# Performance work log

Hardware: AMD Instinct MI355X
Metric: run time of the kernel (lower is better)

The kernel has to match this reference:

```python
import jax, jax.numpy as jnp
import numpy as np

B, S, HID = 2, 2048, 2048
H, HKV, DH = 32, 8, 64
GROUPS = H // HKV
SCALE = DH ** -0.5
ROPE_THETA = 10000.0
NEG_INF = jnp.finfo(jnp.float32).min


def setup_inputs() -> dict:
    key = jax.random.key(0)
    ks = jax.random.split(key, 6)
    hidden_states = jax.random.normal(ks[0], (B, S, HID), dtype=jnp.float32)
    # true rotary embeddings (HF Llama style): inv_freq over half dim, duplicated
    inv_freq = 1.0 / (ROPE_THETA ** (np.arange(0, DH, 2, dtype=np.float32) / DH))
    freqs = np.arange(S, dtype=np.float32)[:, None] * inv_freq[None, :]  # [S, DH/2]
    emb = np.concatenate([freqs, freqs], axis=-1)                        # [S, DH]
    cos = jnp.broadcast_to(jnp.asarray(np.cos(emb), jnp.float32), (B, S, DH))
    sin = jnp.broadcast_to(jnp.asarray(np.sin(emb), jnp.float32), (B, S, DH))
    # additive causal mask [1,1,S,S]
    causal = jnp.tril(jnp.ones((S, S), dtype=bool))
    attention_mask = jnp.where(causal, 0.0, NEG_INF)[None, None].astype(jnp.float32)
    std = 0.02
    Wq = jax.random.normal(ks[1], (H * DH, HID), dtype=jnp.float32) * std
    Wk = jax.random.normal(ks[2], (HKV * DH, HID), dtype=jnp.float32) * std
    Wv = jax.random.normal(ks[3], (HKV * DH, HID), dtype=jnp.float32) * std
    Wo = jax.random.normal(ks[4], (HID, H * DH), dtype=jnp.float32) * std
    return {"hidden_states": hidden_states, "cos": cos, "sin": sin,
            "attention_mask": attention_mask, "Wq": Wq, "Wk": Wk, "Wv": Wv, "Wo": Wo}


def _rotate_half(x):
    x1, x2 = jnp.split(x, 2, axis=-1)
    return jnp.concatenate([-x2, x1], axis=-1)


def reference(hidden_states, cos, sin, attention_mask, Wq, Wk, Wv, Wo):
    b, s, _ = hidden_states.shape
    # projections -> [B, H(kv), S, DH]
    q = (hidden_states @ Wq.T).reshape(b, s, H, DH).transpose(0, 2, 1, 3)
    k = (hidden_states @ Wk.T).reshape(b, s, HKV, DH).transpose(0, 2, 1, 3)
    v = (hidden_states @ Wv.T).reshape(b, s, HKV, DH).transpose(0, 2, 1, 3)
    # RoPE (cos/sin: [B,S,DH] -> broadcast over head axis)
    c = cos[:, None, :, :]
    sn = sin[:, None, :, :]
    q = q * c + _rotate_half(q) * sn
    k = k * c + _rotate_half(k) * sn
    # GQA: repeat kv heads
    k = jnp.repeat(k, GROUPS, axis=1)  # [B,H,S,DH]
    v = jnp.repeat(v, GROUPS, axis=1)
    # eager attention: full [B,H,S,S] scores in memory
    scores = jnp.einsum('bhqd,bhkd->bhqk', q, k) * SCALE + attention_mask[:, :, :, :s]
    attn = jax.nn.softmax(scores, axis=-1)
    out = jnp.einsum('bhqk,bhkd->bhqd', attn, v)
    out = out.transpose(0, 2, 1, 3).reshape(b, s, H * DH)
    return out @ Wo.T
```

## Files before the change

kernel.cpp:

```cpp
#include <hip/hip_runtime.h>
#include <hip/hip_bf16.h>
#include <cstdint>
#include <cstddef>

#define B_    2
#define S_    2048
#define HID_  2048
#define H_    32
#define HKV_  8
#define DH_   64
#define SC2_  0.1803368801111244f

typedef __bf16 bf16;
typedef bf16  bf16x2 __attribute__((ext_vector_type(2)));
typedef bf16  bf16x4 __attribute__((ext_vector_type(4)));
typedef bf16  bf16x8 __attribute__((ext_vector_type(8)));
typedef float f32x4  __attribute__((ext_vector_type(4)));
typedef float f32x16 __attribute__((ext_vector_type(16)));
typedef uint32_t u32x2 __attribute__((ext_vector_type(2)));

typedef __attribute__((address_space(3))) uint32_t  lds_u32_t;
typedef __attribute__((address_space(1))) const uint32_t glob_u32_t;

__device__ __forceinline__ void async16(const void* g, void* l) {
    __builtin_amdgcn_global_load_lds((glob_u32_t*)g, (lds_u32_t*)l, 16, 0, 0);
}

__device__ __forceinline__ bf16x8 cvt8(float4 a, float4 b) {
    bf16x8 r;
    r[0] = (bf16)a.x; r[1] = (bf16)a.y; r[2] = (bf16)a.z; r[3] = (bf16)a.w;
    r[4] = (bf16)b.x; r[5] = (bf16)b.y; r[6] = (bf16)b.z; r[7] = (bf16)b.w;
    return r;
}

__device__ __forceinline__ uint32_t pkbf(float a, float b) {
    bf16x2 t; t[0] = (bf16)a; t[1] = (bf16)b;
    return __builtin_bit_cast(uint32_t, t);
}
__device__ __forceinline__ bf16x8 mk8(uint32_t a, uint32_t b, uint32_t c, uint32_t d) {
    union { uint32_t u[4]; bf16x8 v; } t;
    t.u[0] = a; t.u[1] = b; t.u[2] = c; t.u[3] = d;
    return t.v;
}

__global__ __launch_bounds__(256) void cvt_all_kernel(
    const float* __restrict__ X,  const float* __restrict__ Wq,
    const float* __restrict__ Wk, const float* __restrict__ Wv,
    const float* __restrict__ Wo,
    bf16* __restrict__ Xb,  bf16* __restrict__ Wqb, bf16* __restrict__ Wkb,
    bf16* __restrict__ Wvb, bf16* __restrict__ Wob)
{
    const int i = blockIdx.x * 256 + threadIdx.x;
    const float* src; bf16* dst; int off;
    if (i < 1048576)      { src = X;  dst = Xb;  off = i; }
    else if (i < 1572864) { src = Wq; dst = Wqb; off = i - 1048576; }
    else if (i < 1703936) { src = Wk; dst = Wkb; off = i - 1572864; }
    else if (i < 1835008) { src = Wv; dst = Wvb; off = i - 1703936; }
    else                  { src = Wo; dst = Wob; off = i - 1835008; }
    float4 a = ((const float4*)src)[2 * off];
    float4 b = ((const float4*)src)[2 * off + 1];
    ((bf16x8*)dst)[off] = cvt8(a, b);
}

__global__ __launch_bounds__(256) void gemm_qkv_kernel(
    const bf16* __restrict__ A,
    const bf16* __restrict__ Wqb, const bf16* __restrict__ Wkb,
    const bf16* __restrict__ Wvb,
    const float* __restrict__ cs, const float* __restrict__ sn,
    bf16* __restrict__ Qo, bf16* __restrict__ Ko, bf16* __restrict__ Vt)
{
    __shared__ bf16 a_lds[128 * 64];
    __shared__ bf16 b_lds[128 * 64];

    const int tid  = threadIdx.x;
    const int wave = tid >> 6;
    const int lane = tid & 63;
    const int quad = lane >> 4;
    const int l16  = lane & 15;
    const int wm   = wave >> 1;
    const int wn   = wave & 1;
    const int m0   = blockIdx.x * 128;
    const int n0   = blockIdx.y * 128;

    f32x4 acc[4][4];
    #pragma unroll
    for (int mt = 0; mt < 4; ++mt)
        #pragma unroll
        for (int nt = 0; nt < 4; ++nt)
            acc[mt][nt] = (f32x4){0.f, 0.f, 0.f, 0.f};

    int srow[4], sgcol[4];
    const bf16* browp[4];
    #pragma unroll
    for (int i = 0; i < 4; ++i) {
        const int e = tid * 8 + i * 2048;
        srow[i] = e >> 6;
        const int chunk = (e >> 3) & 7;
        sgcol[i] = (chunk ^ (srow[i] & 7)) << 3;
        const int n = n0 + srow[i];
        browp[i] = (n < 2048) ? (Wqb + (size_t)n * HID_)
                 : (n < 2560) ? (Wkb + (size_t)(n - 2048) * HID_)
                              : (Wvb + (size_t)(n - 2560) * HID_);
    }

    for (int k0 = 0; k0 < HID_; k0 += 64) {
        #pragma unroll
        for (int i = 0; i < 4; ++i) {
            async16(A + (size_t)(m0 + srow[i]) * HID_ + k0 + sgcol[i],
                    &a_lds[tid * 8 + i * 2048]);
            async16(browp[i] + k0 + sgcol[i],
                    &b_lds[tid * 8 + i * 2048]);
        }
        __syncthreads();
        #pragma unroll
        for (int ks = 0; ks < 2; ++ks) {
            bf16x8 af[4], bfr[4];
            #pragma unroll
            for (int mt = 0; mt < 4; ++mt) {
                const int row = wm * 64 + mt * 16 + l16;
                const int c = (ks * 4 + quad) ^ (row & 7);
                af[mt] = *(const bf16x8*)(&a_lds[row * 64 + c * 8]);
            }
            #pragma unroll
            for (int nt = 0; nt < 4; ++nt) {
                const int row = wn * 64 + nt * 16 + l16;
                const int c = (ks * 4 + quad) ^ (row & 7);
                bfr[nt] = *(const bf16x8*)(&b_lds[row * 64 + c * 8]);
            }
            #pragma unroll
            for (int mt = 0; mt < 4; ++mt)
                #pragma unroll
                for (int nt = 0; nt < 4; ++nt)
                    acc[mt][nt] = __builtin_amdgcn_mfma_f32_16x16x32_bf16(
                        af[mt], bfr[nt], acc[mt][nt], 0, 0, 0);
        }
        __syncthreads();
    }

    const int nw = n0 + wn * 64;
    const int d  = l16;
    #pragma unroll
    for (int mt = 0; mt < 4; ++mt) {
        #pragma unroll
        for (int r = 0; r < 4; ++r) {
            const int m  = m0 + wm * 64 + mt * 16 + quad * 4 + r;
            const int bb = m >> 11;
            const int ss = m & (S_ - 1);
            const float v0 = acc[mt][0][r], v1 = acc[mt][1][r];
            const float v2 = acc[mt][2][r], v3 = acc[mt][3][r];
            if (nw < 2048) {
                const int h = nw >> 6;
                bf16* dp = Qo + ((size_t)(bb * H_ + h) * S_ + ss) * DH_;
                const float* cp = cs + ((size_t)bb * S_ + ss) * DH_;
                const float* sp = sn + ((size_t)bb * S_ + ss) * DH_;
                dp[ 0 + d] = (bf16)((v0 * cp[ 0 + d] - v2 * sp[ 0 + d]) * SC2_);
                dp[16 + d] = (bf16)((v1 * cp[16 + d] - v3 * sp[16 + d]) * SC2_);
                dp[32 + d] = (bf16)((v2 * cp[32 + d] + v0 * sp[32 + d]) * SC2_);
                dp[48 + d] = (bf16)((v3 * cp[48 + d] + v1 * sp[48 + d]) * SC2_);
            } else if (nw < 2560) {
                const int h = (nw - 2048) >> 6;
                bf16* dp = Ko + ((size_t)(bb * HKV_ + h) * S_ + ss) * DH_;
                const float* cp = cs + ((size_t)bb * S_ + ss) * DH_;
                const float* sp = sn + ((size_t)bb * S_ + ss) * DH_;
                dp[ 0 + d] = (bf16)(v0 * cp[ 0 + d] - v2 * sp[ 0 + d]);
                dp[16 + d] = (bf16)(v1 * cp[16 + d] - v3 * sp[16 + d]);
                dp[32 + d] = (bf16)(v2 * cp[32 + d] + v0 * sp[32 + d]);
                dp[48 + d] = (bf16)(v3 * cp[48 + d] + v1 * sp[48 + d]);
            } else {
                const int h = (nw - 2560) >> 6;
                bf16* dp = Vt + ((size_t)(bb * HKV_ + h) * DH_) * S_ + ss;
                dp[(size_t)( 0 + d) * S_] = (bf16)v0;
                dp[(size_t)(16 + d) * S_] = (bf16)v1;
                dp[(size_t)(32 + d) * S_] = (bf16)v2;
                dp[(size_t)(48 + d) * S_] = (bf16)v3;
            }
        }
    }
}

__global__ __launch_bounds__(256) void gemm_out_kernel(
    const bf16* __restrict__ A, const bf16* __restrict__ Wb,
    float* __restrict__ Y)
{
    __shared__ bf16 a_lds[128 * 64];
    __shared__ bf16 b_lds[128 * 64];

    const int tid  = threadIdx.x;
    const int wave = tid >> 6;
    const int lane = tid & 63;
    const int quad = lane >> 4;
    const int l16  = lane & 15;
    const int wm   = wave >> 1;
    const int wn   = wave & 1;
    const int m0   = blockIdx.x * 128;
    const int n0   = blockIdx.y * 128;

    f32x4 acc[4][4];
    #pragma unroll
    for (int mt = 0; mt < 4; ++mt)
        #pragma unroll
        for (int nt = 0; nt < 4; ++nt)
            acc[mt][nt] = (f32x4){0.f, 0.f, 0.f, 0.f};

    int srow[4], sgcol[4];
    #pragma unroll
    for (int i = 0; i < 4; ++i) {
        const int e = tid * 8 + i * 2048;
        srow[i] = e >> 6;
        const int chunk = (e >> 3) & 7;
        sgcol[i] = (chunk ^ (srow[i] & 7)) << 3;
    }

    for (int k0 = 0; k0 < HID_; k0 += 64) {
        #pragma unroll
        for (int i = 0; i < 4; ++i) {
            async16(A + (size_t)(m0 + srow[i]) * HID_ + k0 + sgcol[i],
                    &a_lds[tid * 8 + i * 2048]);
            async16(Wb + (size_t)(n0 + srow[i]) * HID_ + k0 + sgcol[i],
                    &b_lds[tid * 8 + i * 2048]);
        }
        __syncthreads();
        #pragma unroll
        for (int ks = 0; ks < 2; ++ks) {
            bf16x8 af[4], bfr[4];
            #pragma unroll
            for (int mt = 0; mt < 4; ++mt) {
                const int row = wm * 64 + mt * 16 + l16;
                const int c = (ks * 4 + quad) ^ (row & 7);
                af[mt] = *(const bf16x8*)(&a_lds[row * 64 + c * 8]);
            }
            #pragma unroll
            for (int nt = 0; nt < 4; ++nt) {
                const int row = wn * 64 + nt * 16 + l16;
                const int c = (ks * 4 + quad) ^ (row & 7);
                bfr[nt] = *(const bf16x8*)(&b_lds[row * 64 + c * 8]);
            }
            #pragma unroll
            for (int mt = 0; mt < 4; ++mt)
                #pragma unroll
                for (int nt = 0; nt < 4; ++nt)
                    acc[mt][nt] = __builtin_amdgcn_mfma_f32_16x16x32_bf16(
                        af[mt], bfr[nt], acc[mt][nt], 0, 0, 0);
        }
        __syncthreads();
    }

    #pragma unroll
    for (int mt = 0; mt < 4; ++mt)
        #pragma unroll
        for (int nt = 0; nt < 4; ++nt)
            #pragma unroll
            for (int r = 0; r < 4; ++r) {
                const int m = m0 + wm * 64 + mt * 16 + quad * 4 + r;
                const int n = n0 + wn * 64 + nt * 16 + l16;
                Y[(size_t)m * HID_ + n] = acc[mt][nt][r];
            }
}

__global__ __launch_bounds__(256) void attn_kernel(
    const bf16* __restrict__ Q, const bf16* __restrict__ K,
    const bf16* __restrict__ Vt, bf16* __restrict__ O)
{
    __shared__ bf16 k_lds[2][64 * 64];
    __shared__ bf16 v_lds[2][64 * 64];

    const int tid  = threadIdx.x;
    const int wave = tid >> 6;
    const int lane = tid & 63;
    const int l32  = lane & 31;
    const int half = lane >> 5;
    const int h  = blockIdx.y;
    const int b  = blockIdx.z;
    const int hkv = h >> 2;

    const bf16* Qg = Q  + (size_t)(b * H_ + h) * S_ * DH_;
    const bf16* Kg = K  + (size_t)(b * HKV_ + hkv) * S_ * DH_;
    const bf16* Vg = Vt + ((size_t)(b * HKV_ + hkv) * DH_) * S_;

    const int srow0  = tid >> 3;
    const int scolsw = ((tid & 7) ^ ((tid >> 3) & 7)) << 3;

    const int p   = blockIdx.x;
    const int st  = (wave < 2) ? p : (31 - p);
    const int qb0 = st * 64 + (wave & 1) * 32;
    const int qa  = qb0 + l32;
    const int nkt = 32 - p;

    bf16x8 qf[4];
    #pragma unroll
    for (int c = 0; c < 4; ++c)
        qf[c] = *(const bf16x8*)(Qg + (size_t)qa * DH_ + c * 16 + half * 8);

    f32x16 o_acc[2];
    #pragma unroll
    for (int dt = 0; dt < 2; ++dt)
        #pragma unroll
        for (int e = 0; e < 16; ++e) o_acc[dt][e] = 0.f;
    float m_i = -1e30f, l_i = 0.f;

    #pragma unroll
    for (int i = 0; i < 2; ++i) {
        const int row = srow0 + i * 32;
        async16(Kg + (size_t)row * DH_ + scolsw, &k_lds[0][tid * 8 + i * 2048]);
        async16(Vg + (size_t)row * S_  + scolsw, &v_lds[0][tid * 8 + i * 2048]);
    }
    __syncthreads();

    for (int kt = 0; kt < nkt; ++kt) {
        if (kt + 1 < nkt) {
            bf16* kb = k_lds[(kt + 1) & 1];
            bf16* vb = v_lds[(kt + 1) & 1];
            #pragma unroll
            for (int i = 0; i < 2; ++i) {
                const int row = srow0 + i * 32;
                async16(Kg + (size_t)((kt + 1) * 64 + row) * DH_ + scolsw,
                        kb + tid * 8 + i * 2048);
                async16(Vg + (size_t)row * S_ + (kt + 1) * 64 + scolsw,
                        vb + tid * 8 + i * 2048);
            }
        }

        if (kt * 64 <= qb0 + 31) {
            const bf16* kb = k_lds[kt & 1];
            const bf16* vb = v_lds[kt & 1];
            const bool act1 = (kt * 64 + 32) <= (qb0 + 31);

            f32x16 s0, s1;
            {
                bf16x8 kf[4];
                #pragma unroll
                for (int c = 0; c < 4; ++c) {
                    const int row = l32;
                    const int col = ((2 * c + half) ^ (row & 7)) << 3;
                    kf[c] = *(const bf16x8*)(kb + row * 64 + col);
                }
                f32x16 a;
                #pragma unroll
                for (int e = 0; e < 16; ++e) a[e] = 0.f;
                #pragma unroll
                for (int c = 0; c < 4; ++c)
                    a = __builtin_amdgcn_mfma_f32_32x32x16_bf16(kf[c], qf[c], a, 0, 0, 0);
                s0 = a;
            }
            if (act1) {
                bf16x8 kf[4];
                #pragma unroll
                for (int c = 0; c < 4; ++c) {
                    const int row = 32 + l32;
                    const int col = ((2 * c + half) ^ (row & 7)) << 3;
                    kf[c] = *(const bf16x8*)(kb + row * 64 + col);
                }
                f32x16 a;
                #pragma unroll
                for (int e = 0; e < 16; ++e) a[e] = 0.f;
                #pragma unroll
                for (int c = 0; c < 4; ++c)
                    a = __builtin_amdgcn_mfma_f32_32x32x16_bf16(kf[c], qf[c], a, 0, 0, 0);
                s1 = a;
            }

            if (!((kt * 64 + 31) <= qb0)) {
                const int qrel = qa - kt * 64 - 4 * half;
                #pragma unroll
                for (int e = 0; e < 16; ++e)
                    if (((e & 3) + 8 * (e >> 2)) > qrel) s0[e] = -1e30f;
            }
            if (act1 && !((kt * 64 + 63) <= qb0)) {
                const int qrel = qa - kt * 64 - 32 - 4 * half;
                #pragma unroll
                for (int e = 0; e < 16; ++e)
                    if (((e & 3) + 8 * (e >> 2)) > qrel) s1[e] = -1e30f;
            }

            float mx = s0[0];
            #pragma unroll
            for (int e = 1; e < 16; ++e) mx = fmaxf(mx, s0[e]);
            if (act1)
                #pragma unroll
                for (int e = 0; e < 16; ++e) mx = fmaxf(mx, s1[e]);
            mx = fmaxf(mx, __shfl_xor(mx, 32));

            float al = 1.f;
            if (!__all(mx <= m_i + 8.f)) {
                const float mn = fmaxf(m_i, mx);
                al = exp2f(m_i - mn);
                m_i = mn;
                #pragma unroll
                for (int dt = 0; dt < 2; ++dt)
                    #pragma unroll
                    for (int e = 0; e < 16; ++e) o_acc[dt][e] *= al;
            }

            float sm = 0.f;
            #pragma unroll
            for (int e = 0; e < 16; ++e) {
                const float pp = exp2f(s0[e] - m_i);
                s0[e] = pp; sm += pp;
            }
            if (act1)
                #pragma unroll
                for (int e = 0; e < 16; ++e) {
                    const float pp = exp2f(s1[e] - m_i);
                    s1[e] = pp; sm += pp;
                }
            sm += __shfl_xor(sm, 32);
            l_i = l_i * al + sm;

            bf16x8 pf[4];
            {
                uint32_t d0 = pkbf(s0[0],  s0[1]),  d1 = pkbf(s0[2],  s0[3]);
                uint32_t d2 = pkbf(s0[4],  s0[5]),  d3 = pkbf(s0[6],  s0[7]);
                uint32_t d4 = pkbf(s0[8],  s0[9]),  d5 = pkbf(s0[10], s0[11]);
                uint32_t d6 = pkbf(s0[12], s0[13]), d7 = pkbf(s0[14], s0[15]);
                u32x2 r02 = __builtin_amdgcn_permlane32_swap(d0, d2, false, false);
                u32x2 r13 = __builtin_amdgcn_permlane32_swap(d1, d3, false, false);
                u32x2 r46 = __builtin_amdgcn_permlane32_swap(d4, d6, false, false);
                u32x2 r57 = __builtin_amdgcn_permlane32_swap(d5, d7, false, false);
                pf[0] = mk8(r02[0], r13[0], r02[1], r13[1]);
                pf[1] = mk8(r46[0], r57[0], r46[1], r57[1]);
            }
            if (act1) {
                uint32_t d0 = pkbf(s1[0],  s1[1]),  d1 = pkbf(s1[2],  s1[3]);
                uint32_t d2 = pkbf(s1[4],  s1[5]),  d3 = pkbf(s1[6],  s1[7]);
                uint32_t d4 = pkbf(s1[8],  s1[9]),  d5 = pkbf(s1[10], s1[11]);
                uint32_t d6 = pkbf(s1[12], s1[13]), d7 = pkbf(s1[14], s1[15]);
                u32x2 r02 = __builtin_amdgcn_permlane32_swap(d0, d2, false, false);
                u32x2 r13 = __builtin_amdgcn_permlane32_swap(d1, d3, false, false);
                u32x2 r46 = __builtin_amdgcn_permlane32_swap(d4, d6, false, false);
                u32x2 r57 = __builtin_amdgcn_permlane32_swap(d5, d7, false, false);
                pf[2] = mk8(r02[0], r13[0], r02[1], r13[1]);
                pf[3] = mk8(r46[0], r57[0], r46[1], r57[1]);
            }

            bf16x8 vf[2][4];
            #pragma unroll
            for (int dt = 0; dt < 2; ++dt)
                #pragma unroll
                for (int c = 0; c < 4; ++c) {
                    const int row = dt * 32 + l32;
                    const int col = ((2 * c + half) ^ (row & 7)) << 3;
                    vf[dt][c] = *(const bf16x8*)(vb + row * 64 + col);
                }

            const int nc = act1 ? 4 : 2;
            #pragma unroll
            for (int c = 0; c < 4; ++c) {
                if (c >= nc) break;
                #pragma unroll
                for (int dt = 0; dt < 2; ++dt)
                    o_acc[dt] = __builtin_amdgcn_mfma_f32_32x32x16_bf16(
                        vf[dt][c], pf[c], o_acc[dt], 0, 0, 0);
            }
        }
        __syncthreads();
    }

    const float inv = 1.f / l_i;
    bf16* op = O + ((size_t)(b * S_ + qa) * H_ + h) * DH_;
    #pragma unroll
    for (int dt = 0; dt < 2; ++dt)
        #pragma unroll
        for (int g = 0; g < 4; ++g) {
            bf16x4 ov;
            #pragma unroll
            for (int r = 0; r < 4; ++r) ov[r] = (bf16)(o_acc[dt][g * 4 + r] * inv);
            *(bf16x4*)(op + dt * 32 + g * 8 + half * 4) = ov;
        }
}

extern "C" void kernel_launch(void* const* d_in, const int* in_sizes, int n_in,
                              void* d_out, int out_size, void* d_ws, size_t ws_size,
                              hipStream_t stream)
{
    const float* X    = (const float*)d_in[0];
    const float* cs   = (const float*)d_in[1];
    const float* sn   = (const float*)d_in[2];
    const float* Wq   = (const float*)d_in[4];
    const float* Wk   = (const float*)d_in[5];
    const float* Wv   = (const float*)d_in[6];
    const float* Wo   = (const float*)d_in[7];
    float* Y          = (float*)d_out;

    bf16* Xb  = (bf16*)d_ws;
    bf16* Wqb = Xb  + (size_t)8388608;
    bf16* Wkb = Wqb + (size_t)4194304;
    bf16* Wvb = Wkb + (size_t)1048576;
    bf16* Wob = Wvb + (size_t)1048576;
    bf16* Qb  = Wob + (size_t)4194304;
    bf16* Kb  = Qb  + (size_t)8388608;
    bf16* Vtb = Kb  + (size_t)2097152;
    bf16* Ob  = Vtb + (size_t)2097152;

    dim3 blk(256);
    cvt_all_kernel<<<dim3(9216), blk, 0, stream>>>(X, Wq, Wk, Wv, Wo,
                                                   Xb, Wqb, Wkb, Wvb, Wob);
    gemm_qkv_kernel<<<dim3(32, 24), blk, 0, stream>>>(Xb, Wqb, Wkb, Wvb,
                                                      cs, sn, Qb, Kb, Vtb);
    attn_kernel<<<dim3(16, H_, B_), blk, 0, stream>>>(Qb, Kb, Vtb, Ob);
    gemm_out_kernel<<<dim3(32, 16), blk, 0, stream>>>(Ob, Wob, Y);
}
```

Before: 418.3 us.

## Restructure attention to 128-row query tiles with 32-key KV tiles

The attention kernel moves from paired 64-row query tiles (front and back halves for causal balance) to one 128-row query tile per block, with each wave owning 32 rows. It streams K/V in 32-key tiles with a repacked V LDS layout, and uses a rotated block-to-tile mapping across heads and batches for load balance. Each K/V tile is now reused by four waves instead of two, and the smaller tiles halve LDS use and cut masked work on the diagonal. In exchange there are twice as many loop iterations and barriers per key range, and scheduling balance now relies on the rotation instead of explicit pairing.

```diff
diff --git a/kernel.cpp b/kernel.cpp
--- a/kernel.cpp
+++ b/kernel.cpp
@@ -261,8 +261,8 @@
     const bf16* __restrict__ Q, const bf16* __restrict__ K,
     const bf16* __restrict__ Vt, bf16* __restrict__ O)
 {
-    __shared__ bf16 k_lds[2][64 * 64];
-    __shared__ bf16 v_lds[2][64 * 64];
+    __shared__ bf16 k_lds[2][32 * 64];
+    __shared__ bf16 v_lds[2][32 * 64];
 
     const int tid  = threadIdx.x;
     const int wave = tid >> 6;
@@ -277,14 +277,16 @@
     const bf16* Kg = K  + (size_t)(b * HKV_ + hkv) * S_ * DH_;
     const bf16* Vg = Vt + ((size_t)(b * HKV_ + hkv) * DH_) * S_;
 
-    const int srow0  = tid >> 3;
-    const int scolsw = ((tid & 7) ^ ((tid >> 3) & 7)) << 3;
-
-    const int p   = blockIdx.x;
-    const int st  = (wave < 2) ? p : (31 - p);
-    const int qb0 = st * 64 + (wave & 1) * 32;
+    const int qt  = 15 - ((blockIdx.x + 4 * ((h >> 4) + 2 * b)) & 15);
+    const int qb0 = qt * 128 + wave * 32;
     const int qa  = qb0 + l32;
-    const int nkt = 32 - p;
+    const int nkt = 4 * qt + 4;
+
+    const int kr = tid >> 3;
+    const int kj = ((tid & 7) ^ (kr & 7)) << 3;
+    const int vj = (tid & 7) ^ (kr & 7);
+    const int vd = kr + 32 * (vj >> 2);
+    const int vs = (vj & 3) * 8;
 
     bf16x8 qf[4];
     #pragma unroll
@@ -298,41 +300,29 @@
         for (int e = 0; e < 16; ++e) o_acc[dt][e] = 0.f;
     float m_i = -1e30f, l_i = 0.f;
 
-    #pragma unroll
-    for (int i = 0; i < 2; ++i) {
-        const int row = srow0 + i * 32;
-        async16(Kg + (size_t)row * DH_ + scolsw, &k_lds[0][tid * 8 + i * 2048]);
-        async16(Vg + (size_t)row * S_  + scolsw, &v_lds[0][tid * 8 + i * 2048]);
-    }
+    async16(Kg + (size_t)kr * DH_ + kj,  &k_lds[0][tid * 8]);
+    async16(Vg + (size_t)vd * S_  + vs,  &v_lds[0][tid * 8]);
     __syncthreads();
 
     for (int kt = 0; kt < nkt; ++kt) {
         if (kt + 1 < nkt) {
-            bf16* kb = k_lds[(kt + 1) & 1];
-            bf16* vb = v_lds[(kt + 1) & 1];
-            #pragma unroll
-            for (int i = 0; i < 2; ++i) {
-                const int row = srow0 + i * 32;
-                async16(Kg + (size_t)((kt + 1) * 64 + row) * DH_ + scolsw,
-                        kb + tid * 8 + i * 2048);
-                async16(Vg + (size_t)row * S_ + (kt + 1) * 64 + scolsw,
-                        vb + tid * 8 + i * 2048);
-            }
-        }
-
-        if (kt * 64 <= qb0 + 31) {
+            async16(Kg + (size_t)((kt + 1) * 32 + kr) * DH_ + kj,
+                    &k_lds[(kt + 1) & 1][tid * 8]);
+            async16(Vg + (size_t)vd * S_ + (kt + 1) * 32 + vs,
+                    &v_lds[(kt + 1) & 1][tid * 8]);
+        }
+
+        if (kt * 32 <= qb0 + 31) {
             const bf16* kb = k_lds[kt & 1];
             const bf16* vb = v_lds[kt & 1];
-            const bool act1 = (kt * 64 + 32) <= (qb0 + 31);
-
-            f32x16 s0, s1;
+
+            f32x16 s0;
             {
                 bf16x8 kf[4];
                 #pragma unroll
                 for (int c = 0; c < 4; ++c) {
-                    const int row = l32;
-                    const int col = ((2 * c + half) ^ (row & 7)) << 3;
-                    kf[c] = *(const bf16x8*)(kb + row * 64 + col);
+                    const int ch = (2 * c + half) ^ (l32 & 7);
+                    kf[c] = *(const bf16x8*)(kb + l32 * 64 + ch * 8);
                 }
                 f32x16 a;
                 #pragma unroll
@@ -342,42 +332,17 @@
                     a = __builtin_amdgcn_mfma_f32_32x32x16_bf16(kf[c], qf[c], a, 0, 0, 0);
                 s0 = a;
             }
-            if (act1) {
-                bf16x8 kf[4];
-                #pragma unroll
-                for (int c = 0; c < 4; ++c) {
-                    const int row = 32 + l32;
-                    const int col = ((2 * c + half) ^ (row & 7)) << 3;
-                    kf[c] = *(const bf16x8*)(kb + row * 64 + col);
-                }
-                f32x16 a;
-                #pragma unroll
-                for (int e = 0; e < 16; ++e) a[e] = 0.f;
-                #pragma unroll
-                for (int c = 0; c < 4; ++c)
-                    a = __builtin_amdgcn_mfma_f32_32x32x16_bf16(kf[c], qf[c], a, 0, 0, 0);
-                s1 = a;
-            }
-
-            if (!((kt * 64 + 31) <= qb0)) {
-                const int qrel = qa - kt * 64 - 4 * half;
+
+            if (!((kt * 32 + 31) <= qb0)) {
+                const int qrel = qa - kt * 32 - 4 * half;
                 #pragma unroll
                 for (int e = 0; e < 16; ++e)
                     if (((e & 3) + 8 * (e >> 2)) > qrel) s0[e] = -1e30f;
             }
-            if (act1 && !((kt * 64 + 63) <= qb0)) {
-                const int qrel = qa - kt * 64 - 32 - 4 * half;
-                #pragma unroll
-                for (int e = 0; e < 16; ++e)
-                    if (((e & 3) + 8 * (e >> 2)) > qrel) s1[e] = -1e30f;
-            }
 
             float mx = s0[0];
             #pragma unroll
             for (int e = 1; e < 16; ++e) mx = fmaxf(mx, s0[e]);
-            if (act1)
-                #pragma unroll
-                for (int e = 0; e < 16; ++e) mx = fmaxf(mx, s1[e]);
             mx = fmaxf(mx, __shfl_xor(mx, 32));
 
             float al = 1.f;
@@ -397,16 +362,10 @@
                 const float pp = exp2f(s0[e] - m_i);
                 s0[e] = pp; sm += pp;
             }
-            if (act1)
-                #pragma unroll
-                for (int e = 0; e < 16; ++e) {
-                    const float pp = exp2f(s1[e] - m_i);
-                    s1[e] = pp; sm += pp;
-                }
             sm += __shfl_xor(sm, 32);
             l_i = l_i * al + sm;
 
-            bf16x8 pf[4];
+            bf16x8 pf[2];
             {
                 uint32_t d0 = pkbf(s0[0],  s0[1]),  d1 = pkbf(s0[2],  s0[3]);
                 uint32_t d2 = pkbf(s0[4],  s0[5]),  d3 = pkbf(s0[6],  s0[7]);
@@ -419,38 +378,22 @@
                 pf[0] = mk8(r02[0], r13[0], r02[1], r13[1]);
                 pf[1] = mk8(r46[0], r57[0], r46[1], r57[1]);
             }
-            if (act1) {
-                uint32_t d0 = pkbf(s1[0],  s1[1]),  d1 = pkbf(s1[2],  s1[3]);
-                uint32_t d2 = pkbf(s1[4],  s1[5]),  d3 = pkbf(s1[6],  s1[7]);
-                uint32_t d4 = pkbf(s1[8],  s1[9]),  d5 = pkbf(s1[10], s1[11]);
-                uint32_t d6 = pkbf(s1[12], s1[13]), d7 = pkbf(s1[14], s1[15]);
-                u32x2 r02 = __builtin_amdgcn_permlane32_swap(d0, d2, false, false);
-                u32x2 r13 = __builtin_amdgcn_permlane32_swap(d1, d3, false, false);
-                u32x2 r46 = __builtin_amdgcn_permlane32_swap(d4, d6, false, false);
-                u32x2 r57 = __builtin_amdgcn_permlane32_swap(d5, d7, false, false);
-                pf[2] = mk8(r02[0], r13[0], r02[1], r13[1]);
-                pf[3] = mk8(r46[0], r57[0], r46[1], r57[1]);
-            }
-
-            bf16x8 vf[2][4];
+
+            bf16x8 vf[2][2];
             #pragma unroll
             for (int dt = 0; dt < 2; ++dt)
                 #pragma unroll
-                for (int c = 0; c < 4; ++c) {
-                    const int row = dt * 32 + l32;
-                    const int col = ((2 * c + half) ^ (row & 7)) << 3;
-                    vf[dt][c] = *(const bf16x8*)(vb + row * 64 + col);
+                for (int c = 0; c < 2; ++c) {
+                    const int ch = (dt * 4 + 2 * c + half) ^ (l32 & 7);
+                    vf[dt][c] = *(const bf16x8*)(vb + l32 * 64 + ch * 8);
                 }
 
-            const int nc = act1 ? 4 : 2;
-            #pragma unroll
-            for (int c = 0; c < 4; ++c) {
-                if (c >= nc) break;
+            #pragma unroll
+            for (int c = 0; c < 2; ++c)
                 #pragma unroll
                 for (int dt = 0; dt < 2; ++dt)
                     o_acc[dt] = __builtin_amdgcn_mfma_f32_32x32x16_bf16(
                         vf[dt][c], pf[c], o_acc[dt], 0, 0, 0);
-            }
         }
         __syncthreads();
     }
```

Result: faster. 391.6 us (-6.4%).
